# Optimization experiments

Measured on AMD Instinct MI355X. Metric: run time of the kernel, lower is better.

The kernel has to match this reference:

```python
import jax, jax.numpy as jnp
import numpy as np

B, S, D = 4, 4096, 1024
DFF = 4 * D
ACTIVE = 1024  # ceil(S * 0.25)


def setup_inputs() -> dict:
    key = jax.random.key(0)
    ks = jax.random.split(key, 4)
    x = jax.random.normal(ks[0], (B, S, D), dtype=jnp.float32)
    rw = jax.random.normal(ks[1], (D,), dtype=jnp.float32) * 0.02
    rb = jnp.zeros((1,), dtype=jnp.float32)
    w1 = jax.random.normal(ks[2], (D, DFF), dtype=jnp.float32) * 0.02
    b1 = jnp.zeros((DFF,), dtype=jnp.float32)
    w2 = jax.random.normal(ks[3], (DFF, D), dtype=jnp.float32) * 0.02
    b2 = jnp.zeros((D,), dtype=jnp.float32)
    return {"x": x, "rw": rw, "rb": rb, "w1": w1, "b1": b1,
            "w2": w2, "b2": b2, "active_tokens": ACTIVE}


def reference(x, rw, rb, w1, b1, w2, b2, active_tokens):
    b, s, d = x.shape
    # router: Linear(n_embd, 1) -> [B, S] scores
    scores = jnp.einsum('bsd,d->bs', x, rw) + rb[0]
    # top-k tokens per batch row
    _, idx = jax.lax.top_k(scores, active_tokens)          # [B, K] int32
    sel = jnp.take_along_axis(x, idx[..., None], axis=1)   # [B, K, D]
    # dense MLP on selected tokens (exact GELU as in torch nn.GELU)
    h = jax.nn.gelu(jnp.einsum('bkd,df->bkf', sel, w1) + b1, approximate=False)
    out = jnp.einsum('bkf,fd->bkd', h, w2) + b2            # [B, K, D]
    # sigmoid gate from router scores of selected tokens
    gates = jax.nn.sigmoid(jnp.take_along_axis(scores, idx, axis=1))  # [B, K]
    out = out * gates[..., None]
    # scatter back into zeros at selected positions
    flat_idx = (idx + jnp.arange(b, dtype=idx.dtype)[:, None] * s).reshape(-1)
    flat_out = jnp.zeros((b * s, d), dtype=out.dtype)
    flat_out = flat_out.at[flat_idx].set(out.reshape(-1, d))
    return flat_out.reshape(b, s, d)
```

## Files before the change

### kernel.cpp

```cpp
#include <hip/hip_runtime.h>
#include <hip/hip_bf16.h>
#include <cstdint>
#include <cstddef>

#define Bz 4
#define Sz 4096
#define Dz 1024
#define DFFz 4096
#define KACT 1024

typedef __bf16 bf16;
typedef __attribute__((ext_vector_type(8))) __bf16 bf16x8;
typedef __attribute__((ext_vector_type(4))) __bf16 bf16x4;
typedef __attribute__((ext_vector_type(4))) float f32x4;

__device__ __forceinline__ void async16(const void* g, void* l) {
  __builtin_amdgcn_global_load_lds(
      (const __attribute__((address_space(1))) void*)g,
      (__attribute__((address_space(3))) void*)l, 16, 0, 0);
}

__global__ __launch_bounds__(256) void prep_k(const float* __restrict__ x,
                                              const float* __restrict__ rw,
                                              const float* __restrict__ rb,
                                              float* __restrict__ scores,
                                              float4* __restrict__ out4,
                                              const float* __restrict__ w1,
                                              bf16* __restrict__ w1T,
                                              const float* __restrict__ w2,
                                              bf16* __restrict__ w2T) {
  __shared__ float t[32][33];
  const int bid = blockIdx.x;
  const int tid = threadIdx.x;
  if (bid < 4096) {
    int row = bid * 4 + (tid >> 6);
    int lane = tid & 63;
    const float4* xr = (const float4*)(x + (size_t)row * Dz);
    const float4* wr = (const float4*)rw;
    float acc = 0.f;
#pragma unroll
    for (int i = 0; i < 4; ++i) {
      float4 a = xr[lane + i * 64];
      float4 w = wr[lane + i * 64];
      acc += a.x * w.x + a.y * w.y + a.z * w.z + a.w * w.w;
    }
#pragma unroll
    for (int d = 32; d; d >>= 1) acc += __shfl_down(acc, d, 64);
    if (lane == 0) scores[row] = acc + rb[0];
    float4* o = out4 + (size_t)bid * 4 * (Dz / 4);
    const float4 z = make_float4(0.f, 0.f, 0.f, 0.f);
#pragma unroll
    for (int i = 0; i < 4; ++i) o[tid + i * 256] = z;
  } else {
    const float* in; bf16* outp; int R, C, bx, by;
    if (bid < 8192) {
      in = w1; outp = w1T; R = Dz; C = DFFz;
      bx = (bid - 4096) & 127; by = (bid - 4096) >> 7;
    } else {
      in = w2; outp = w2T; R = DFFz; C = Dz;
      bx = (bid - 8192) & 31; by = (bid - 8192) >> 5;
    }
    int c0 = bx * 32, r0 = by * 32;
    int tx = tid & 31, ty = tid >> 5;
#pragma unroll
    for (int i = 0; i < 32; i += 8) t[ty + i][tx] = in[(size_t)(r0 + ty + i) * C + c0 + tx];
    __syncthreads();
#pragma unroll
    for (int i = 0; i < 32; i += 8)
      outp[(size_t)(c0 + ty + i) * R + r0 + tx] = (bf16)t[tx][ty + i];
  }
}

__global__ __launch_bounds__(256) void select_gather_k(
    const float* __restrict__ x, const float* __restrict__ scores,
    int* __restrict__ sel_idx, float* __restrict__ gates, bf16* __restrict__ Xsel) {
  int b = blockIdx.x >> 8;
  int s0 = (blockIdx.x & 255) * 16;
  __shared__ float sc[Sz];
  __shared__ int red[16][4];
  __shared__ int rk[16];
  const int tid = threadIdx.x;
  const int wave = tid >> 6, lane = tid & 63;
  const float* srow = scores + (size_t)b * Sz;
#pragma unroll
  for (int i = 0; i < 4; ++i)
    ((float4*)sc)[tid + i * 256] = ((const float4*)srow)[tid + i * 256];
  __syncthreads();
  float mine[16];
#pragma unroll
  for (int j = 0; j < 16; ++j) mine[j] = sc[s0 + j];
  int cnt[16] = {};
  for (int t = tid; t < Sz; t += 256) {
    float o = sc[t];
#pragma unroll
    for (int j = 0; j < 16; ++j)
      cnt[j] += (o > mine[j]) || (o == mine[j] && t < s0 + j);
  }
#pragma unroll
  for (int j = 0; j < 16; ++j) {
    int c = cnt[j];
#pragma unroll
    for (int d = 32; d; d >>= 1) c += __shfl_down(c, d, 64);
    if (lane == 0) red[j][wave] = c;
  }
  __syncthreads();
  if (tid < 16) {
    int rank = red[tid][0] + red[tid][1] + red[tid][2] + red[tid][3];
    rk[tid] = rank;
    if (rank < KACT) {
      int m = b * KACT + rank;
      sel_idx[m] = s0 + tid;
      gates[m] = 1.f / (1.f + expf(-sc[s0 + tid]));
    }
  }
  __syncthreads();
#pragma unroll
  for (int j = 0; j < 16; ++j) {
    int rank = rk[j];
    if (rank >= KACT) continue;
    int m = b * KACT + rank;
    float4 v = ((const float4*)(x + ((size_t)b * Sz + s0 + j) * Dz))[tid];
    bf16x4 o = {(bf16)v.x, (bf16)v.y, (bf16)v.z, (bf16)v.w};
    ((bf16x4*)(Xsel + (size_t)m * Dz))[tid] = o;
  }
}


#define BAR_VM4 asm volatile("s_waitcnt vmcnt(4) lgkmcnt(0)\n\ts_barrier" ::: "memory")
#define BAR_VM0 asm volatile("s_waitcnt vmcnt(0) lgkmcnt(0)\n\ts_barrier" ::: "memory")

#define STG(AS, BS, T)                                                        \
  {                                                                           \
    size_t ko = (size_t)(T) * 64;                                             \
    async16(pa0 + ko, (char*)AS + Ld0);                                       \
    async16(pa1 + ko, (char*)AS + Ld1);                                       \
    async16(pb0 + ko, (char*)BS + Ld0);                                       \
    async16(pb1 + ko, (char*)BS + Ld1);                                       \
  }

#define GBODY(ARD, BRD, AST, BST, T, DOSTAGE, BARK)                           \
  {                                                                           \
    if (DOSTAGE) { STG(AST, BST, (T) + 2) }                                   \
    bf16x8 af[4], bfr[4];                                                     \
    const char* a_ = (const char*)ARD;                                        \
    const char* b_ = (const char*)BRD;                                        \
    _Pragma("unroll") for (int i = 0; i < 4; ++i) {                           \
      af[i] = *(const bf16x8*)(a_ + aoff[i]);                                 \
      bfr[i] = *(const bf16x8*)(b_ + boff[i]);                                \
    }                                                                         \
    __builtin_amdgcn_s_setprio(1);                                            \
    _Pragma("unroll") for (int mi = 0; mi < 4; ++mi)                          \
      _Pragma("unroll") for (int ni = 0; ni < 4; ++ni)                        \
        acc[mi][ni] = __builtin_amdgcn_mfma_f32_16x16x32_bf16(                \
            af[mi], bfr[ni], acc[mi][ni], 0, 0, 0);                           \
    __builtin_amdgcn_s_setprio(0);                                            \
    if ((BARK) == 0) { BAR_VM4; }                                             \
    else if ((BARK) == 1) { BAR_VM0; }                                        \
  }

#define GSETUP(APTR, BPTR, KV, KOFFB)                                         \
  const int tid = threadIdx.x;                                                \
  const int wave = tid >> 6, lane = tid & 63;                                 \
  const int quad = lane >> 4, l16 = lane & 15;                                \
  const int wm = (wave >> 1) * 64, wn = (wave & 1) * 64;                      \
  const int Ld0 = tid * 16, Ld1 = 4096 + tid * 16;                            \
  const int q0 = Ld0 ^ (((Ld0 >> 7) & 3) << 4);                               \
  const int q1 = Ld1 ^ (((Ld1 >> 7) & 3) << 4);                               \
  const char* pa0 = (const char*)(APTR) +                                     \
      ((size_t)(m0 + (q0 >> 6)) * (KV)) * 2 + (KOFFB) + (q0 & 63);            \
  const char* pa1 = (const char*)(APTR) +                                     \
      ((size_t)(m0 + (q1 >> 6)) * (KV)) * 2 + (KOFFB) + (q1 & 63);            \
  const char* pb0 = (const char*)(BPTR) +                                     \
      ((size_t)(n0 + (q0 >> 6)) * (KV)) * 2 + (KOFFB) + (q0 & 63);            \
  const char* pb1 = (const char*)(BPTR) +                                     \
      ((size_t)(n0 + (q1 >> 6)) * (KV)) * 2 + (KOFFB) + (q1 & 63);            \
  int aoff[4], boff[4];                                                       \
  _Pragma("unroll") for (int i = 0; i < 4; ++i) {                             \
    int ra = wm + i * 16 + l16;                                               \
    int oa = ra * 64 + quad * 16;                                             \
    aoff[i] = oa ^ (((ra >> 1) & 3) << 4);                                    \
    int rb = wn + i * 16 + l16;                                               \
    int ob = rb * 64 + quad * 16;                                             \
    boff[i] = ob ^ (((rb >> 1) & 3) << 4);                                    \
  }                                                                           \
  f32x4 acc[4][4] = {};

__global__ __launch_bounds__(256) void gemm1_k(const bf16* __restrict__ A,
                                               const bf16* __restrict__ Bt,
                                               const float* __restrict__ bias,
                                               bf16* __restrict__ H) {
  __shared__ __align__(16) bf16 A0[4096], A1[4096], A2[4096];
  __shared__ __align__(16) bf16 B0[4096], B1[4096], B2[4096];
  const int orig = blockIdx.y * 32 + blockIdx.x;
  const int wgid = (orig & 7) * 128 + (orig >> 3);
  const int m0 = (wgid >> 5) * 128, n0 = (wgid & 31) * 128;
  GSETUP(A, Bt, Dz, 0)
  STG(A0, B0, 0)
  STG(A1, B1, 1)
  BAR_VM4;
  for (int tt = 0; tt < 10; ++tt) {
    const int t0 = tt * 3;
    GBODY(A0, B0, A2, B2, t0 + 0, 1, 0)
    GBODY(A1, B1, A0, B0, t0 + 1, 1, 0)
    GBODY(A2, B2, A1, B1, t0 + 2, 1, 0)
  }
  GBODY(A0, B0, A0, B0, 30, 0, 1)
  GBODY(A1, B1, A0, B0, 31, 0, 2)
#pragma unroll
  for (int mi = 0; mi < 4; ++mi) {
    int mb = m0 + wm + mi * 16 + quad * 4;
#pragma unroll
    for (int ni = 0; ni < 4; ++ni) {
      int n = n0 + wn + ni * 16 + l16;
      float bn = bias[n];
#pragma unroll
      for (int r = 0; r < 4; ++r) {
        float z = acc[mi][ni][r] + bn;
        float g = 0.5f * z * (1.f + erff(z * 0.70710678118654752f));
        H[(size_t)(mb + r) * DFFz + n] = (bf16)g;
      }
    }
  }
}

__global__ __launch_bounds__(256) void gemm2_k(const bf16* __restrict__ A,
                                               const bf16* __restrict__ Bt,
                                               const float* __restrict__ b2,
                                               const int* __restrict__ sel_idx,
                                               const float* __restrict__ gates,
                                               float* __restrict__ out) {
  __shared__ __align__(16) bf16 A0[4096], A1[4096], A2[4096];
  __shared__ __align__(16) bf16 B0[4096], B1[4096], B2[4096];
  const int orig = blockIdx.y * 8 + blockIdx.x;
  const int wgid = (orig & 7) * 32 + (orig >> 3);
  const int m0 = (wgid >> 3) * 128, n0 = (wgid & 7) * 128;
  GSETUP(A, Bt, DFFz, (size_t)blockIdx.z * 2048 * 2)
  STG(A0, B0, 0)
  STG(A1, B1, 1)
  BAR_VM4;
  for (int tt = 0; tt < 20; ++tt) {
    const int t0 = tt * 3;
    GBODY(A0, B0, A2, B2, t0 + 0, 1, 0)
    GBODY(A1, B1, A0, B0, t0 + 1, 1, 0)
    GBODY(A2, B2, A1, B1, t0 + 2, 1, 0)
  }
  GBODY(A0, B0, A2, B2, 60, 1, 0)
  GBODY(A1, B1, A0, B0, 61, 1, 0)
  GBODY(A2, B2, A0, B0, 62, 0, 1)
  GBODY(A0, B0, A0, B0, 63, 0, 2)
  const bool addb = (blockIdx.z == 0);
#pragma unroll
  for (int mi = 0; mi < 4; ++mi) {
#pragma unroll
    for (int r = 0; r < 4; ++r) {
      int m = m0 + wm + mi * 16 + quad * 4 + r;
      int b = m >> 10;
      int s = sel_idx[m];
      float g = gates[m];
      float* orow = out + ((size_t)b * Sz + s) * Dz;
#pragma unroll
      for (int ni = 0; ni < 4; ++ni) {
        int n = n0 + wn + ni * 16 + l16;
        float v = acc[mi][ni][r] + (addb ? b2[n] : 0.f);
        atomicAdd(&orow[n], v * g);
      }
    }
  }
}

extern "C" void kernel_launch(void* const* d_in, const int* in_sizes, int n_in,
                              void* d_out, int out_size, void* d_ws, size_t ws_size,
                              hipStream_t stream) {
  (void)in_sizes; (void)n_in; (void)out_size; (void)ws_size;
  const float* x  = (const float*)d_in[0];
  const float* rw = (const float*)d_in[1];
  const float* rb = (const float*)d_in[2];
  const float* w1 = (const float*)d_in[3];
  const float* b1 = (const float*)d_in[4];
  const float* w2 = (const float*)d_in[5];
  const float* b2 = (const float*)d_in[6];
  float* out = (float*)d_out;

  char* ws = (char*)d_ws;
  float* scores = (float*)ws;  ws += (size_t)Bz * Sz * 4;
  int*   sel_idx = (int*)ws;   ws += (size_t)Bz * KACT * 4;
  float* gates = (float*)ws;   ws += (size_t)Bz * KACT * 4;
  bf16*  w2T = (bf16*)ws;      ws += (size_t)Dz * DFFz * 2;
  bf16*  H = (bf16*)ws;        ws += (size_t)Bz * KACT * DFFz * 2;
  bf16*  w1T = (bf16*)ws;      ws += (size_t)DFFz * Dz * 2;
  bf16*  Xsel = (bf16*)ws;     ws += (size_t)Bz * KACT * Dz * 2;

  prep_k<<<3 * 4096, 256, 0, stream>>>(x, rw, rb, scores, (float4*)out, w1, w1T, w2, w2T);
  select_gather_k<<<Bz * (Sz / 16), 256, 0, stream>>>(x, scores, sel_idx, gates, Xsel);
  gemm1_k<<<dim3(32, 32), 256, 0, stream>>>(Xsel, w1T, b1, H);
  gemm2_k<<<dim3(8, 32, 2), 256, 0, stream>>>(H, w2T, b2, sel_idx, gates, out);
}
```

Baseline: 306.4 us.

## Switch GEMMs to K=64 tiles with double buffering and wider LDS swizzle

Both GEMM kernels now stage 128x64 bf16 tiles per step instead of 128x32, using two LDS buffers instead of three. The XOR swizzle widens from 4 to 8 chunks to match the 128-byte rows. Each iteration issues twice the MFMAs per barrier, halving the number of barriers and waits. The trade-off is shallower prefetch: each step waits with vmcnt(0) for the next tile, so less memory latency is hidden.

New measurement: 296.3 us. 3.3% less time.

```diff
diff --git a/kernel.cpp b/kernel.cpp
--- a/kernel.cpp
+++ b/kernel.cpp
@@ -126,36 +126,40 @@
 }
 
 
-#define BAR_VM4 asm volatile("s_waitcnt vmcnt(4) lgkmcnt(0)\n\ts_barrier" ::: "memory")
 #define BAR_VM0 asm volatile("s_waitcnt vmcnt(0) lgkmcnt(0)\n\ts_barrier" ::: "memory")
 
 #define STG(AS, BS, T)                                                        \
   {                                                                           \
-    size_t ko = (size_t)(T) * 64;                                             \
-    async16(pa0 + ko, (char*)AS + Ld0);                                       \
-    async16(pa1 + ko, (char*)AS + Ld1);                                       \
-    async16(pb0 + ko, (char*)BS + Ld0);                                       \
-    async16(pb1 + ko, (char*)BS + Ld1);                                       \
-  }
-
-#define GBODY(ARD, BRD, AST, BST, T, DOSTAGE, BARK)                           \
+    size_t ko_ = (size_t)(T) * 128;                                           \
+    async16(pa0 + ko_, (char*)AS + Ld0);                                      \
+    async16(pa1 + ko_, (char*)AS + Ld1);                                      \
+    async16(pa2 + ko_, (char*)AS + Ld2);                                      \
+    async16(pa3 + ko_, (char*)AS + Ld3);                                      \
+    async16(pb0 + ko_, (char*)BS + Ld0);                                      \
+    async16(pb1 + ko_, (char*)BS + Ld1);                                      \
+    async16(pb2 + ko_, (char*)BS + Ld2);                                      \
+    async16(pb3 + ko_, (char*)BS + Ld3);                                      \
+  }
+
+#define GB(ARD, BRD, AST, BST, T, DOSTAGE, DOBAR)                             \
   {                                                                           \
-    if (DOSTAGE) { STG(AST, BST, (T) + 2) }                                   \
-    bf16x8 af[4], bfr[4];                                                     \
+    if (DOSTAGE) { STG(AST, BST, (T) + 1) }                                   \
     const char* a_ = (const char*)ARD;                                        \
     const char* b_ = (const char*)BRD;                                        \
-    _Pragma("unroll") for (int i = 0; i < 4; ++i) {                           \
-      af[i] = *(const bf16x8*)(a_ + aoff[i]);                                 \
-      bfr[i] = *(const bf16x8*)(b_ + boff[i]);                                \
-    }                                                                         \
+    bf16x8 af[2][4], bfr[2][4];                                               \
+    _Pragma("unroll") for (int kc = 0; kc < 2; ++kc)                          \
+      _Pragma("unroll") for (int i = 0; i < 4; ++i) {                         \
+        af[kc][i] = *(const bf16x8*)(a_ + aoff[kc][i]);                       \
+        bfr[kc][i] = *(const bf16x8*)(b_ + boff[kc][i]);                      \
+      }                                                                       \
     __builtin_amdgcn_s_setprio(1);                                            \
-    _Pragma("unroll") for (int mi = 0; mi < 4; ++mi)                          \
-      _Pragma("unroll") for (int ni = 0; ni < 4; ++ni)                        \
-        acc[mi][ni] = __builtin_amdgcn_mfma_f32_16x16x32_bf16(                \
-            af[mi], bfr[ni], acc[mi][ni], 0, 0, 0);                           \
+    _Pragma("unroll") for (int kc = 0; kc < 2; ++kc)                          \
+      _Pragma("unroll") for (int mi = 0; mi < 4; ++mi)                        \
+        _Pragma("unroll") for (int ni = 0; ni < 4; ++ni)                      \
+          acc[mi][ni] = __builtin_amdgcn_mfma_f32_16x16x32_bf16(              \
+              af[kc][mi], bfr[kc][ni], acc[mi][ni], 0, 0, 0);                 \
     __builtin_amdgcn_s_setprio(0);                                            \
-    if ((BARK) == 0) { BAR_VM4; }                                             \
-    else if ((BARK) == 1) { BAR_VM0; }                                        \
+    if (DOBAR) { BAR_VM0; }                                                   \
   }
 
 #define GSETUP(APTR, BPTR, KV, KOFFB)                                         \
@@ -163,49 +167,58 @@
   const int wave = tid >> 6, lane = tid & 63;                                 \
   const int quad = lane >> 4, l16 = lane & 15;                                \
   const int wm = (wave >> 1) * 64, wn = (wave & 1) * 64;                      \
-  const int Ld0 = tid * 16, Ld1 = 4096 + tid * 16;                            \
-  const int q0 = Ld0 ^ (((Ld0 >> 7) & 3) << 4);                               \
-  const int q1 = Ld1 ^ (((Ld1 >> 7) & 3) << 4);                               \
+  const int Ld0 = tid * 16, Ld1 = Ld0 + 4096, Ld2 = Ld0 + 8192,               \
+            Ld3 = Ld0 + 12288;                                                \
+  const int q0 = Ld0 ^ (((Ld0 >> 7) & 7) << 4);                               \
+  const int q1 = Ld1 ^ (((Ld1 >> 7) & 7) << 4);                               \
+  const int q2 = Ld2 ^ (((Ld2 >> 7) & 7) << 4);                               \
+  const int q3 = Ld3 ^ (((Ld3 >> 7) & 7) << 4);                               \
   const char* pa0 = (const char*)(APTR) +                                     \
-      ((size_t)(m0 + (q0 >> 6)) * (KV)) * 2 + (KOFFB) + (q0 & 63);            \
+      ((size_t)(m0 + (q0 >> 7)) * (KV)) * 2 + (KOFFB) + (q0 & 127);           \
   const char* pa1 = (const char*)(APTR) +                                     \
-      ((size_t)(m0 + (q1 >> 6)) * (KV)) * 2 + (KOFFB) + (q1 & 63);            \
+      ((size_t)(m0 + (q1 >> 7)) * (KV)) * 2 + (KOFFB) + (q1 & 127);           \
+  const char* pa2 = (const char*)(APTR) +                                     \
+      ((size_t)(m0 + (q2 >> 7)) * (KV)) * 2 + (KOFFB) + (q2 & 127);           \
+  const char* pa3 = (const char*)(APTR) +                                     \
+      ((size_t)(m0 + (q3 >> 7)) * (KV)) * 2 + (KOFFB) + (q3 & 127);           \
   const char* pb0 = (const char*)(BPTR) +                                     \
-      ((size_t)(n0 + (q0 >> 6)) * (KV)) * 2 + (KOFFB) + (q0 & 63);            \
+      ((size_t)(n0 + (q0 >> 7)) * (KV)) * 2 + (KOFFB) + (q0 & 127);           \
   const char* pb1 = (const char*)(BPTR) +                                     \
-      ((size_t)(n0 + (q1 >> 6)) * (KV)) * 2 + (KOFFB) + (q1 & 63);            \
-  int aoff[4], boff[4];                                                       \
-  _Pragma("unroll") for (int i = 0; i < 4; ++i) {                             \
-    int ra = wm + i * 16 + l16;                                               \
-    int oa = ra * 64 + quad * 16;                                             \
-    aoff[i] = oa ^ (((ra >> 1) & 3) << 4);                                    \
-    int rb = wn + i * 16 + l16;                                               \
-    int ob = rb * 64 + quad * 16;                                             \
-    boff[i] = ob ^ (((rb >> 1) & 3) << 4);                                    \
-  }                                                                           \
+      ((size_t)(n0 + (q1 >> 7)) * (KV)) * 2 + (KOFFB) + (q1 & 127);           \
+  const char* pb2 = (const char*)(BPTR) +                                     \
+      ((size_t)(n0 + (q2 >> 7)) * (KV)) * 2 + (KOFFB) + (q2 & 127);           \
+  const char* pb3 = (const char*)(BPTR) +                                     \
+      ((size_t)(n0 + (q3 >> 7)) * (KV)) * 2 + (KOFFB) + (q3 & 127);           \
+  int aoff[2][4], boff[2][4];                                                 \
+  _Pragma("unroll") for (int kc = 0; kc < 2; ++kc)                            \
+    _Pragma("unroll") for (int i = 0; i < 4; ++i) {                           \
+      int ra = wm + i * 16 + l16;                                             \
+      int oa = ra * 128 + kc * 64 + quad * 16;                                \
+      aoff[kc][i] = oa ^ ((ra & 7) << 4);                                     \
+      int rb = wn + i * 16 + l16;                                             \
+      int ob = rb * 128 + kc * 64 + quad * 16;                                \
+      boff[kc][i] = ob ^ ((rb & 7) << 4);                                     \
+    }                                                                         \
   f32x4 acc[4][4] = {};
 
 __global__ __launch_bounds__(256) void gemm1_k(const bf16* __restrict__ A,
                                                const bf16* __restrict__ Bt,
                                                const float* __restrict__ bias,
                                                bf16* __restrict__ H) {
-  __shared__ __align__(16) bf16 A0[4096], A1[4096], A2[4096];
-  __shared__ __align__(16) bf16 B0[4096], B1[4096], B2[4096];
+  __shared__ __align__(16) bf16 A0[8192], A1[8192];
+  __shared__ __align__(16) bf16 B0[8192], B1[8192];
   const int orig = blockIdx.y * 32 + blockIdx.x;
   const int wgid = (orig & 7) * 128 + (orig >> 3);
   const int m0 = (wgid >> 5) * 128, n0 = (wgid & 31) * 128;
   GSETUP(A, Bt, Dz, 0)
   STG(A0, B0, 0)
-  STG(A1, B1, 1)
-  BAR_VM4;
-  for (int tt = 0; tt < 10; ++tt) {
-    const int t0 = tt * 3;
-    GBODY(A0, B0, A2, B2, t0 + 0, 1, 0)
-    GBODY(A1, B1, A0, B0, t0 + 1, 1, 0)
-    GBODY(A2, B2, A1, B1, t0 + 2, 1, 0)
-  }
-  GBODY(A0, B0, A0, B0, 30, 0, 1)
-  GBODY(A1, B1, A0, B0, 31, 0, 2)
+  BAR_VM0;
+  for (int tt = 0; tt < 7; ++tt) {
+    GB(A0, B0, A1, B1, 2 * tt + 0, 1, 1)
+    GB(A1, B1, A0, B0, 2 * tt + 1, 1, 1)
+  }
+  GB(A0, B0, A1, B1, 14, 1, 1)
+  GB(A1, B1, A0, B0, 15, 0, 0)
 #pragma unroll
   for (int mi = 0; mi < 4; ++mi) {
     int mb = m0 + wm + mi * 16 + quad * 4;
@@ -229,25 +242,20 @@
                                                const int* __restrict__ sel_idx,
                                                const float* __restrict__ gates,
                                                float* __restrict__ out) {
-  __shared__ __align__(16) bf16 A0[4096], A1[4096], A2[4096];
-  __shared__ __align__(16) bf16 B0[4096], B1[4096], B2[4096];
+  __shared__ __align__(16) bf16 A0[8192], A1[8192];
+  __shared__ __align__(16) bf16 B0[8192], B1[8192];
   const int orig = blockIdx.y * 8 + blockIdx.x;
   const int wgid = (orig & 7) * 32 + (orig >> 3);
   const int m0 = (wgid >> 3) * 128, n0 = (wgid & 7) * 128;
   GSETUP(A, Bt, DFFz, (size_t)blockIdx.z * 2048 * 2)
   STG(A0, B0, 0)
-  STG(A1, B1, 1)
-  BAR_VM4;
-  for (int tt = 0; tt < 20; ++tt) {
-    const int t0 = tt * 3;
-    GBODY(A0, B0, A2, B2, t0 + 0, 1, 0)
-    GBODY(A1, B1, A0, B0, t0 + 1, 1, 0)
-    GBODY(A2, B2, A1, B1, t0 + 2, 1, 0)
-  }
-  GBODY(A0, B0, A2, B2, 60, 1, 0)
-  GBODY(A1, B1, A0, B0, 61, 1, 0)
-  GBODY(A2, B2, A0, B0, 62, 0, 1)
-  GBODY(A0, B0, A0, B0, 63, 0, 2)
+  BAR_VM0;
+  for (int tt = 0; tt < 15; ++tt) {
+    GB(A0, B0, A1, B1, 2 * tt + 0, 1, 1)
+    GB(A1, B1, A0, B0, 2 * tt + 1, 1, 1)
+  }
+  GB(A0, B0, A1, B1, 30, 1, 1)
+  GB(A1, B1, A0, B0, 31, 0, 0)
   const bool addb = (blockIdx.z == 0);
 #pragma unroll
   for (int mi = 0; mi < 4; ++mi) {
```
